# Kernel optimization log

Hardware: AMD Instinct MI355X
Metric: run time of the kernel (lower is better)

## Reference

```python
import jax, jax.numpy as jnp
import numpy as np
from jax import lax

D_MODEL = 1024; N_HEADS = 16; D_FF = 4096
D_INNER = 2048; D_STATE = 16; D_CONV = 4; DT_RANK = 64
B = 4; T = 1024; TF = 512
HD = D_MODEL // N_HEADS


def setup_inputs() -> dict:
    key = jax.random.key(0)
    ks = jax.random.split(key, 24)
    r = lambda i, shape, s=0.02: jax.random.normal(ks[i], shape, jnp.float32) * s
    lengths = jnp.array([512, 384, 448, 320])
    styled_mask = jnp.arange(TF)[None, :] < lengths[:, None]  # True = valid
    inp = {
        'x': jax.random.normal(ks[0], (B, T, D_MODEL), jnp.float32),
        'styled_frames': jax.random.normal(ks[1], (B, TF, D_MODEL), jnp.float32),
        'styled_mask': styled_mask,
        'ln1_g': jnp.ones((D_MODEL,)), 'ln1_b': jnp.zeros((D_MODEL,)),
        'ln2_g': jnp.ones((D_MODEL,)), 'ln2_b': jnp.zeros((D_MODEL,)),
        'ln3_g': jnp.ones((D_MODEL,)), 'ln3_b': jnp.zeros((D_MODEL,)),
        'm_in_w': r(2, (D_MODEL, 2 * D_INNER)),
        'm_conv_w': r(3, (D_INNER, D_CONV), 0.1),
        'm_conv_b': jnp.zeros((D_INNER,)),
        'm_xproj_w': r(4, (D_INNER, DT_RANK + 2 * D_STATE)),
        'm_dt_w': r(5, (DT_RANK, D_INNER), 0.1),
        'm_dt_b': jnp.full((D_INNER,), -4.6),  # softplus -> dt ~ 0.01
        'm_A_log': jnp.log(jnp.broadcast_to(jnp.arange(1, D_STATE + 1, dtype=jnp.float32), (D_INNER, D_STATE))),
        'm_D': jnp.ones((D_INNER,)),
        'm_out_w': r(6, (D_INNER, D_MODEL)),
        'attn_in_w': r(7, (3 * D_MODEL, D_MODEL)),
        'attn_in_b': jnp.zeros((3 * D_MODEL,)),
        'attn_out_w': r(8, (D_MODEL, D_MODEL)),
        'attn_out_b': jnp.zeros((D_MODEL,)),
        'ff_w1': r(9, (D_MODEL, D_FF)),
        'ff_b1': jnp.zeros((D_FF,)),
        'ff_w2': r(10, (D_FF, D_MODEL)),
        'ff_b2': jnp.zeros((D_MODEL,)),
    }
    return inp


def _layer_norm(x, g, b):
    m = x.mean(-1, keepdims=True)
    v = ((x - m) ** 2).mean(-1, keepdims=True)
    return (x - m) / jnp.sqrt(v + 1e-5) * g + b


def _mamba(h, m_in_w, m_conv_w, m_conv_b, m_xproj_w, m_dt_w, m_dt_b, m_A_log, m_D, m_out_w):
    xz = h @ m_in_w                                   # (B,T,2*d_inner)
    xm, z = jnp.split(xz, 2, axis=-1)
    # causal depthwise conv1d
    xt = jnp.pad(xm.transpose(0, 2, 1), ((0, 0), (0, 0), (D_CONV - 1, 0)))  # (B,d_inner,T+pad)
    xc = lax.conv_general_dilated(xt, m_conv_w[:, None, :], (1,), 'VALID',
                                  feature_group_count=D_INNER,
                                  dimension_numbers=('NCH', 'OIH', 'NCH'))
    xc = jax.nn.silu(xc + m_conv_b[None, :, None]).transpose(0, 2, 1)       # (B,T,d_inner)
    x_dbl = xc @ m_xproj_w
    dt, Bs, Cs = jnp.split(x_dbl, [DT_RANK, DT_RANK + D_STATE], axis=-1)
    dt = jax.nn.softplus(dt @ m_dt_w + m_dt_b)        # (B,T,d_inner)
    A = -jnp.exp(m_A_log)                             # (d_inner,d_state)

    def step(hs, inp):
        dt_t, B_t, C_t, u_t = inp                     # (B,d_inner),(B,d_state),(B,d_state),(B,d_inner)
        dA = jnp.exp(dt_t[:, :, None] * A)            # (B,d_inner,d_state)
        hs = dA * hs + dt_t[:, :, None] * B_t[:, None, :] * u_t[:, :, None]
        y = jnp.einsum('bds,bs->bd', hs, C_t)
        return hs, y

    h0 = jnp.zeros((xc.shape[0], D_INNER, D_STATE), xc.dtype)
    inputs = (dt.transpose(1, 0, 2), Bs.transpose(1, 0, 2), Cs.transpose(1, 0, 2), xc.transpose(1, 0, 2))
    hT, ys = lax.scan(step, h0, inputs)
    y = ys.transpose(1, 0, 2) + xc * m_D
    y = y * jax.nn.silu(z)
    return y @ m_out_w, hT


def _cross_attn(q_in, kv_in, valid_mask, in_w, in_b, out_w, out_b):
    d = D_MODEL
    q = q_in @ in_w[:d].T + in_b[:d]
    k = kv_in @ in_w[d:2 * d].T + in_b[d:2 * d]
    v = kv_in @ in_w[2 * d:].T + in_b[2 * d:]
    q = q.reshape(q.shape[0], q.shape[1], N_HEADS, HD)
    k = k.reshape(k.shape[0], k.shape[1], N_HEADS, HD)
    v = v.reshape(v.shape[0], v.shape[1], N_HEADS, HD)
    scores = jnp.einsum('bqhd,bkhd->bhqk', q, k) / np.sqrt(HD)
    scores = jnp.where(valid_mask[:, None, None, :], scores, jnp.finfo(scores.dtype).min)
    attn = jax.nn.softmax(scores, axis=-1)
    o = jnp.einsum('bhqk,bkhd->bqhd', attn, v).reshape(q_in.shape)
    return o @ out_w.T + out_b


def reference(x, styled_frames, styled_mask,
              ln1_g, ln1_b, ln2_g, ln2_b, ln3_g, ln3_b,
              m_in_w, m_conv_w, m_conv_b, m_xproj_w, m_dt_w, m_dt_b, m_A_log, m_D, m_out_w,
              attn_in_w, attn_in_b, attn_out_w, attn_out_b,
              ff_w1, ff_b1, ff_w2, ff_b2):
    h = _layer_norm(x, ln1_g, ln1_b)
    h_mamba, new_state = _mamba(h, m_in_w, m_conv_w, m_conv_b, m_xproj_w, m_dt_w, m_dt_b, m_A_log, m_D, m_out_w)
    x = x + h_mamba
    h = _layer_norm(x, ln2_g, ln2_b)
    x = x + _cross_attn(h, styled_frames, styled_mask, attn_in_w, attn_in_b, attn_out_w, attn_out_b)
    h = _layer_norm(x, ln3_g, ln3_b)
    ff = jax.nn.gelu(h @ ff_w1 + ff_b1, approximate=False) @ ff_w2 + ff_b2
    x = x + ff
    return x, new_state
```

## Files before the change

### kernel.cpp

```cpp
#include <hip/hip_runtime.h>
#include <hip/hip_bf16.h>
#include <cstdint>

using bf16 = __hip_bfloat16;

typedef __attribute__((ext_vector_type(8))) short short8;
typedef __attribute__((ext_vector_type(4))) float floatx4;

__device__ __forceinline__ float b2f(bf16 h) { return __bfloat162float(h); }
__device__ __forceinline__ bf16 f2b(float f) { return __float2bfloat16(f); }
__device__ __forceinline__ float uitf(unsigned u) { union { unsigned u; float f; } c; c.u = u; return c.f; }

__device__ __forceinline__ void async16(const bf16* g, bf16* l) {
    __builtin_amdgcn_global_load_lds(
        (const __attribute__((address_space(1))) uint32_t*)(const void*)g,
        (__attribute__((address_space(3))) uint32_t*)(void*)l, 16, 0, 0);
}

__global__ void lens_flag_kernel(const unsigned char* __restrict__ mask,
                                 const unsigned int* __restrict__ ln1g_raw,
                                 int* __restrict__ hdr) {
    __shared__ int cnt[4];
    int tid = threadIdx.x;
    if (tid < 4) cnt[tid] = 0;
    __syncthreads();
    unsigned char b0 = mask[0], b1 = mask[1];
    int width = (b1 == 0) ? 4 : ((b0 == 1) ? 1 : 2);
    if (width == 4) {
        const unsigned int* m = (const unsigned int*)mask;
        for (int i = tid; i < 2048; i += 256) if (m[i] != 0u) atomicAdd(&cnt[i >> 9], 1);
    } else if (width == 2) {
        const unsigned short* m = (const unsigned short*)mask;
        for (int i = tid; i < 2048; i += 256) if (m[i] != 0u) atomicAdd(&cnt[i >> 9], 1);
    } else {
        for (int i = tid; i < 2048; i += 256) if (mask[i] != 0u) atomicAdd(&cnt[i >> 9], 1);
    }
    __syncthreads();
    if (tid < 4) hdr[tid] = cnt[tid];
    if (tid == 4) hdr[4] = (ln1g_raw[0] == 0x3F800000u) ? 1 : 0;
}

__global__ void convert_kernel(const void* __restrict__ src, bf16* __restrict__ dst, int n,
                               const int* __restrict__ flagp) {
    int i = blockIdx.x * 256 + threadIdx.x;
    if (i >= n) return;
    if (*flagp) dst[i] = f2b(((const float*)src)[i]);
    else        dst[i] = ((const bf16*)src)[i];
}

struct SmallSrcs { const void* p[15]; };
__global__ void convert_smalls_kernel(SmallSrcs s, bf16* __restrict__ dst,
                                      const int* __restrict__ flagp) {
    const int ends[16] = {0, 1024, 2048, 3072, 4096, 5120, 6144, 14336, 16384, 18432,
                          51200, 53248, 56320, 57344, 61440, 62464};
    int i = blockIdx.x * 256 + threadIdx.x;
    if (i >= 62464) return;
    int seg = 0;
    #pragma unroll
    for (int k = 1; k < 16; ++k) if (i >= ends[k]) seg = k;
    int local = i - ends[seg];
    const void* sp = s.p[seg];
    if (*flagp) dst[i] = f2b(((const float*)sp)[local]);
    else        dst[i] = ((const bf16*)sp)[local];
}

__global__ void transpose_any(const void* __restrict__ src, bf16* __restrict__ dst,
                              int R, int C, const int* __restrict__ flagp) {
    __shared__ bf16 tile[32][33];
    bool f32 = (*flagp != 0);
    int bx = blockIdx.x * 32, by = blockIdx.y * 32;
    int tx = threadIdx.x;
    for (int i = threadIdx.y; i < 32; i += 8) {
        int y = by + i, x = bx + tx;
        if (y < R && x < C) {
            size_t idx = (size_t)y * C + x;
            tile[i][tx] = f32 ? f2b(((const float*)src)[idx]) : ((const bf16*)src)[idx];
        }
    }
    __syncthreads();
    for (int i = threadIdx.y; i < 32; i += 8) {
        int yo = bx + i, xo = by + tx;
        if (yo < C && xo < R) dst[(size_t)yo * R + xo] = tile[tx][i];
    }
}

__global__ void vtrans_kernel(const bf16* __restrict__ v, bf16* __restrict__ vt) {
    __shared__ bf16 t[32][33];
    int kc = blockIdx.x * 32, dc = blockIdx.y * 32;
    int bh = blockIdx.z; int b = bh >> 4, h = bh & 15;
    int tx = threadIdx.x;
    for (int i = threadIdx.y; i < 32; i += 8)
        t[i][tx] = v[(size_t)(b * 512 + kc + i) * 1024 + h * 64 + dc + tx];
    __syncthreads();
    for (int i = threadIdx.y; i < 32; i += 8)
        vt[(size_t)(bh * 64 + dc + i) * 512 + kc + tx] = t[tx][i];
}

__global__ __launch_bounds__(256) void ln_kernel(const bf16* __restrict__ x, const bf16* __restrict__ g,
                                                 const bf16* __restrict__ bb, bf16* __restrict__ out) {
    int row = blockIdx.x, tid = threadIdx.x;
    const bf16* xr = x + (size_t)row * 1024;
    float v[4];
    {
        uint2 raw = *(const uint2*)(xr + tid * 4);
        v[0] = uitf(raw.x << 16); v[1] = uitf(raw.x & 0xffff0000u);
        v[2] = uitf(raw.y << 16); v[3] = uitf(raw.y & 0xffff0000u);
    }
    float sum = v[0] + v[1] + v[2] + v[3];
    float sq = v[0]*v[0] + v[1]*v[1] + v[2]*v[2] + v[3]*v[3];
    for (int off = 32; off; off >>= 1) { sum += __shfl_xor(sum, off); sq += __shfl_xor(sq, off); }
    __shared__ float wsm[8];
    int wave = tid >> 6;
    if ((tid & 63) == 0) { wsm[wave * 2] = sum; wsm[wave * 2 + 1] = sq; }
    __syncthreads();
    sum = wsm[0] + wsm[2] + wsm[4] + wsm[6];
    sq  = wsm[1] + wsm[3] + wsm[5] + wsm[7];
    float mean = sum * (1.f / 1024.f);
    float var = sq * (1.f / 1024.f) - mean * mean;
    float rstd = rsqrtf(var + 1e-5f);
    bf16* orow = out + (size_t)row * 1024;
    #pragma unroll
    for (int c = 0; c < 4; ++c) {
        int col = tid * 4 + c;
        orow[col] = f2b((v[c] - mean) * rstd * b2f(g[col]) + b2f(bb[col]));
    }
}

__global__ __launch_bounds__(256) void gemm_bt(
    const bf16* __restrict__ A, int lda,
    const bf16* __restrict__ Bt, int ldb,
    void* __restrict__ Cp, int ldc, int c_f32,
    int M, int N, int K,
    const bf16* __restrict__ bias,
    const bf16* __restrict__ res, int ldres,
    int act)
{
    __shared__ __align__(16) bf16 As[2][128 * 32];
    __shared__ __align__(16) bf16 Bs[2][128 * 32];
    const int tid = threadIdx.x;
    const int lane = tid & 63;
    const int wave = tid >> 6;
    const int wr = (wave >> 1) * 64;
    const int wc = (wave & 1) * 64;
    const int lrow = lane & 15;
    const int quad = lane >> 4;
    const int m0 = blockIdx.y * 128;
    const int n0 = blockIdx.x * 128;

    const int r0 = tid >> 2;
    const int c0 = (tid & 3) << 3;

    floatx4 acc[4][4];
    #pragma unroll
    for (int i = 0; i < 4; ++i)
        #pragma unroll
        for (int j = 0; j < 4; ++j) acc[i][j] = (floatx4){0.f, 0.f, 0.f, 0.f};

    const int n1 = n0 + r0, n2 = n0 + r0 + 64;
    const bool fullN = (n0 + 128 <= N);
    const bool bok1 = n1 < N, bok2 = n2 < N;
    const int4 z4 = {0, 0, 0, 0};

    const bf16* Ag1 = A + (size_t)(m0 + r0) * lda + c0;
    const bf16* Ag2 = A + (size_t)(m0 + r0 + 64) * lda + c0;
    const bf16* Bg1 = Bt + (size_t)n1 * ldb + c0;
    const bf16* Bg2 = Bt + (size_t)n2 * ldb + c0;

    auto stage = [&](int buf, int k0) {
        bf16* AsW = &As[buf][tid * 8];
        bf16* BsW = &Bs[buf][tid * 8];
        async16(Ag1 + k0, AsW);
        async16(Ag2 + k0, AsW + 64 * 32);
        if (fullN) {
            async16(Bg1 + k0, BsW);
            async16(Bg2 + k0, BsW + 64 * 32);
        } else {
            *(int4*)BsW              = bok1 ? *(const int4*)(Bg1 + k0) : z4;
            *(int4*)(BsW + 64 * 32)  = bok2 ? *(const int4*)(Bg2 + k0) : z4;
        }
    };

    const int nt = K >> 5;
    stage(0, 0);
    __syncthreads();
    for (int t = 0; t < nt; ++t) {
        const int cur = t & 1;
        if (t + 1 < nt) stage(cur ^ 1, (t + 1) << 5);
        short8 af[4], bfr[4];
        #pragma unroll
        for (int i = 0; i < 4; ++i) af[i]  = *(const short8*)&As[cur][(wr + i * 16 + lrow) * 32 + quad * 8];
        #pragma unroll
        for (int j = 0; j < 4; ++j) bfr[j] = *(const short8*)&Bs[cur][(wc + j * 16 + lrow) * 32 + quad * 8];
        #pragma unroll
        for (int i = 0; i < 4; ++i)
            #pragma unroll
            for (int j = 0; j < 4; ++j)
                acc[i][j] = __builtin_amdgcn_mfma_f32_16x16x32_bf16(af[i], bfr[j], acc[i][j], 0, 0, 0);
        __syncthreads();
    }

    #pragma unroll
    for (int j = 0; j < 4; ++j) {
        int col = n0 + wc + j * 16 + lrow;
        if (col >= N) continue;
        float bv = bias ? b2f(bias[col]) : 0.f;
        #pragma unroll
        for (int i = 0; i < 4; ++i) {
            #pragma unroll
            for (int r = 0; r < 4; ++r) {
                int row = m0 + wr + i * 16 + quad * 4 + r;
                float v = acc[i][j][r] + bv;
                if (act == 1)      v = 0.5f * v * (1.f + erff(v * 0.70710678118f));
                else if (act == 2) v = (v > 15.f) ? v : log1pf(__expf(v));
                if (res) v += b2f(res[(size_t)row * ldres + col]);
                if (c_f32) ((float*)Cp)[(size_t)row * ldc + col] = v;
                else       ((bf16*)Cp)[(size_t)row * ldc + col] = f2b(v);
            }
        }
    }
}

__global__ __launch_bounds__(256) void conv_silu_kernel(const bf16* __restrict__ xz, const bf16* __restrict__ cw,
                                                        const bf16* __restrict__ cb, bf16* __restrict__ xc) {
    int idx = blockIdx.x * 256 + threadIdx.x;
    int d = idx & 2047;
    int row = idx >> 11;
    int t = row & 1023;
    int base = row - t;
    float acc = b2f(cb[d]);
    #pragma unroll
    for (int j = 0; j < 4; ++j) {
        int tt = t - 3 + j;
        if (tt >= 0) acc += b2f(xz[(size_t)(base + tt) * 4096 + d]) * b2f(cw[d * 4 + j]);
    }
    xc[idx] = f2b(acc * (1.f / (1.f + __expf(-acc))));
}

__global__ __launch_bounds__(256) void scan_part1(
    const bf16* __restrict__ dt, const bf16* __restrict__ xc, const bf16* __restrict__ xdbl,
    const bf16* __restrict__ A_log, float* __restrict__ Pb, float* __restrict__ qb)
{
    __shared__ float smB[128][20];
    const int tid = threadIdx.x;
    const int dgrp = blockIdx.x, c = blockIdx.y, b = blockIdx.z;
    const int dl = tid >> 1, sh = tid & 1;
    const int d = (dgrp << 7) + dl;
    const size_t rowbase = (size_t)b * 1024 + (size_t)c * 128;

    {
        int r = tid >> 1, q = tid & 1;
        short8 raw = *(const short8*)(xdbl + (rowbase + r) * 96 + 64 + q * 8);
        #pragma unroll
        for (int j = 0; j < 8; ++j) smB[r][q * 8 + j] = b2f(((const bf16*)&raw)[j]);
    }
    __syncthreads();

    float A2[8], h[8];
    #pragma unroll
    for (int s = 0; s < 8; ++s) {
        A2[s] = -__expf(b2f(A_log[d * 16 + sh * 8 + s])) * 1.44269504f;
        h[s] = 0.f;
    }
    float dtsum = 0.f;
    const bf16* dtp = dt + rowbase * 2048 + d;
    const bf16* up  = xc + rowbase * 2048 + d;
    for (int tc = 0; tc < 128; tc += 8) {
        float dtv[8], uv[8];
        #pragma unroll
        for (int i = 0; i < 8; ++i) {
            dtv[i] = b2f(dtp[(size_t)(tc + i) * 2048]);
            uv[i]  = b2f(up[(size_t)(tc + i) * 2048]);
        }
        #pragma unroll
        for (int i = 0; i < 8; ++i) {
            float dtf = dtv[i];
            dtsum += dtf;
            float w = dtf * uv[i];
            float4 B0 = *(const float4*)&smB[tc + i][sh * 8];
            float4 B1 = *(const float4*)&smB[tc + i][sh * 8 + 4];
            float Bv[8] = {B0.x, B0.y, B0.z, B0.w, B1.x, B1.y, B1.z, B1.w};
            #pragma unroll
            for (int s = 0; s < 8; ++s) {
                float e = __builtin_amdgcn_exp2f(dtf * A2[s]);
                h[s] = fmaf(e, h[s], w * Bv[s]);
            }
        }
    }
    size_t gid = ((size_t)(b * 2048 + d) * 16 + sh * 8) + (size_t)c * 131072;
    float Pv[8];
    #pragma unroll
    for (int s = 0; s < 8; ++s) Pv[s] = __builtin_amdgcn_exp2f(A2[s] * dtsum);
    *(float4*)(Pb + gid)     = *(float4*)&Pv[0];
    *(float4*)(Pb + gid + 4) = *(float4*)&Pv[4];
    *(float4*)(qb + gid)     = *(float4*)&h[0];
    *(float4*)(qb + gid + 4) = *(float4*)&h[4];
}

__global__ __launch_bounds__(256) void scan_stitch(
    const float* __restrict__ Pb, const float* __restrict__ qb,
    float* __restrict__ hs, float* __restrict__ state_out)
{
    int gid = blockIdx.x * 256 + threadIdx.x;
    float h = 0.f;
    #pragma unroll
    for (int c = 0; c < 8; ++c) {
        hs[gid + c * 131072] = h;
        h = Pb[gid + c * 131072] * h + qb[gid + c * 131072];
    }
    state_out[gid] = h;
}

__global__ __launch_bounds__(256) void scan_part3(
    const bf16* __restrict__ dt, const bf16* __restrict__ xc, const bf16* __restrict__ xdbl,
    const bf16* __restrict__ xz, const bf16* __restrict__ A_log, const bf16* __restrict__ Dp,
    const float* __restrict__ hs, bf16* __restrict__ ymul)
{
    __shared__ float smBC[128][36];
    const int tid = threadIdx.x;
    const int dgrp = blockIdx.x, c = blockIdx.y, b = blockIdx.z;
    const int dl = tid >> 1, sh = tid & 1;
    const int d = (dgrp << 7) + dl;
    const size_t rowbase = (size_t)b * 1024 + (size_t)c * 128;

    {
        int r = tid >> 1, q = tid & 1;
        const bf16* src = xdbl + (rowbase + r) * 96 + 64 + q * 16;
        short8 raw0 = *(const short8*)src;
        short8 raw1 = *(const short8*)(src + 8);
        #pragma unroll
        for (int j = 0; j < 8; ++j) {
            smBC[r][q * 16 + j]     = b2f(((const bf16*)&raw0)[j]);
            smBC[r][q * 16 + 8 + j] = b2f(((const bf16*)&raw1)[j]);
        }
    }
    __syncthreads();

    float A2[8], h[8];
    size_t gid = ((size_t)(b * 2048 + d) * 16 + sh * 8) + (size_t)c * 131072;
    {
        float4 h0 = *(const float4*)(hs + gid);
        float4 h1 = *(const float4*)(hs + gid + 4);
        h[0] = h0.x; h[1] = h0.y; h[2] = h0.z; h[3] = h0.w;
        h[4] = h1.x; h[5] = h1.y; h[6] = h1.z; h[7] = h1.w;
    }
    #pragma unroll
    for (int s = 0; s < 8; ++s)
        A2[s] = -__expf(b2f(A_log[d * 16 + sh * 8 + s])) * 1.44269504f;
    const float Dv = b2f(Dp[d]);
    const bf16* dtp = dt + rowbase * 2048 + d;
    const bf16* up  = xc + rowbase * 2048 + d;
    const bf16* zp  = xz + rowbase * 4096 + 2048 + d;
    bf16* yp = ymul + rowbase * 2048 + d;
    for (int tc = 0; tc < 128; tc += 8) {
        float dtv[8], uv[8], zv[8];
        #pragma unroll
        for (int i = 0; i < 8; ++i) {
            dtv[i] = b2f(dtp[(size_t)(tc + i) * 2048]);
            uv[i]  = b2f(up[(size_t)(tc + i) * 2048]);
            zv[i]  = b2f(zp[(size_t)(tc + i) * 4096]);
        }
        #pragma unroll
        for (int i = 0; i < 8; ++i) {
            float dtf = dtv[i], uf = uv[i];
            float w = dtf * uf;
            float4 B0 = *(const float4*)&smBC[tc + i][sh * 8];
            float4 B1 = *(const float4*)&smBC[tc + i][sh * 8 + 4];
            float4 C0 = *(const float4*)&smBC[tc + i][16 + sh * 8];
            float4 C1 = *(const float4*)&smBC[tc + i][16 + sh * 8 + 4];
            float Bv[8] = {B0.x, B0.y, B0.z, B0.w, B1.x, B1.y, B1.z, B1.w};
            float Cv[8] = {C0.x, C0.y, C0.z, C0.w, C1.x, C1.y, C1.z, C1.w};
            float y = 0.f;
            #pragma unroll
            for (int s = 0; s < 8; ++s) {
                float e = __builtin_amdgcn_exp2f(dtf * A2[s]);
                h[s] = fmaf(e, h[s], w * Bv[s]);
                y = fmaf(h[s], Cv[s], y);
            }
            y += __shfl_xor(y, 1);
            float z = zv[i];
            float sig = __builtin_amdgcn_rcpf(1.f + __builtin_amdgcn_exp2f(-1.44269504f * z));
            float o = (y + uf * Dv) * (z * sig);
            if (sh == 0) yp[(size_t)(tc + i) * 2048] = f2b(o);
        }
    }
}

__global__ __launch_bounds__(256) void attn_mfma(
    const bf16* __restrict__ qb, const bf16* __restrict__ kb, const bf16* __restrict__ vt,
    const int* __restrict__ lens, bf16* __restrict__ ob)
{
    const int qt = blockIdx.x, h = blockIdx.y, b = blockIdx.z;
    const int tid = threadIdx.x;
    const int wave = tid >> 6;
    const int lane = tid & 63;
    const int l15 = lane & 15;
    const int quad = lane >> 4;
    const int len = lens[b];

    __shared__ __align__(16) bf16 Ps[32][520];
    __shared__ float red_sh[4][32];

    short8 aq[2][2];
    const bf16* qbase = qb + (size_t)(b * 1024 + qt * 32 + l15) * 1024 + h * 64 + quad * 8;
    #pragma unroll
    for (int mt = 0; mt < 2; ++mt)
        #pragma unroll
        for (int ks = 0; ks < 2; ++ks)
            aq[mt][ks] = *(const short8*)(qbase + (size_t)mt * 16 * 1024 + ks * 32);

    floatx4 accs[2][8];
    #pragma unroll
    for (int mt = 0; mt < 2; ++mt)
        #pragma unroll
        for (int nt = 0; nt < 8; ++nt) accs[mt][nt] = (floatx4){0.f, 0.f, 0.f, 0.f};

    const bf16* kbase = kb + (size_t)(b * 512 + wave * 128 + l15) * 1024 + h * 64 + quad * 8;
    #pragma unroll
    for (int nt = 0; nt < 8; ++nt) {
        short8 bk0 = *(const short8*)(kbase + (size_t)nt * 16 * 1024);
        short8 bk1 = *(const short8*)(kbase + (size_t)nt * 16 * 1024 + 32);
        #pragma unroll
        for (int mt = 0; mt < 2; ++mt) {
            accs[mt][nt] = __builtin_amdgcn_mfma_f32_16x16x32_bf16(aq[mt][0], bk0, accs[mt][nt], 0, 0, 0);
            accs[mt][nt] = __builtin_amdgcn_mfma_f32_16x16x32_bf16(aq[mt][1], bk1, accs[mt][nt], 0, 0, 0);
        }
    }

    float pm[2][4];
    #pragma unroll
    for (int mt = 0; mt < 2; ++mt)
        #pragma unroll
        for (int r = 0; r < 4; ++r) pm[mt][r] = -1e30f;
    #pragma unroll
    for (int mt = 0; mt < 2; ++mt)
        #pragma unroll
        for (int nt = 0; nt < 8; ++nt) {
            int col = wave * 128 + nt * 16 + l15;
            bool ok = col < len;
            #pragma unroll
            for (int r = 0; r < 4; ++r) {
                float s = ok ? accs[mt][nt][r] * 0.125f : -1e30f;
                accs[mt][nt][r] = s;
                pm[mt][r] = fmaxf(pm[mt][r], s);
            }
        }
    #pragma unroll
    for (int off = 1; off < 16; off <<= 1)
        #pragma unroll
        for (int mt = 0; mt < 2; ++mt)
            #pragma unroll
            for (int r = 0; r < 4; ++r) pm[mt][r] = fmaxf(pm[mt][r], __shfl_xor(pm[mt][r], off));
    if (l15 == 0)
        #pragma unroll
        for (int mt = 0; mt < 2; ++mt)
            #pragma unroll
            for (int r = 0; r < 4; ++r) red_sh[wave][mt * 16 + quad * 4 + r] = pm[mt][r];
    __syncthreads();
    float rowmax[2][4];
    #pragma unroll
    for (int mt = 0; mt < 2; ++mt)
        #pragma unroll
        for (int r = 0; r < 4; ++r) {
            int row = mt * 16 + quad * 4 + r;
            rowmax[mt][r] = fmaxf(fmaxf(red_sh[0][row], red_sh[1][row]),
                                  fmaxf(red_sh[2][row], red_sh[3][row]));
        }
    __syncthreads();

    float ps[2][4] = {{0.f, 0.f, 0.f, 0.f}, {0.f, 0.f, 0.f, 0.f}};
    #pragma unroll
    for (int mt = 0; mt < 2; ++mt)
        #pragma unroll
        for (int nt = 0; nt < 8; ++nt)
            #pragma unroll
            for (int r = 0; r < 4; ++r) {
                float p = __expf(accs[mt][nt][r] - rowmax[mt][r]);
                accs[mt][nt][r] = p;
                ps[mt][r] += p;
            }
    #pragma unroll
    for (int off = 1; off < 16; off <<= 1)
        #pragma unroll
        for (int mt = 0; mt < 2; ++mt)
            #pragma unroll
            for (int r = 0; r < 4; ++r) ps[mt][r] += __shfl_xor(ps[mt][r], off);
    if (l15 == 0)
        #pragma unroll
        for (int mt = 0; mt < 2; ++mt)
            #pragma unroll
            for (int r = 0; r < 4; ++r) red_sh[wave][mt * 16 + quad * 4 + r] = ps[mt][r];
    #pragma unroll
    for (int mt = 0; mt < 2; ++mt)
        #pragma unroll
        for (int nt = 0; nt < 8; ++nt)
            #pragma unroll
            for (int r = 0; r < 4; ++r)
                Ps[mt * 16 + quad * 4 + r][wave * 128 + nt * 16 + l15] = f2b(accs[mt][nt][r]);
    __syncthreads();
    float rowsum[2][4];
    #pragma unroll
    for (int mt = 0; mt < 2; ++mt)
        #pragma unroll
        for (int r = 0; r < 4; ++r) {
            int row = mt * 16 + quad * 4 + r;
            rowsum[mt][r] = red_sh[0][row] + red_sh[1][row] + red_sh[2][row] + red_sh[3][row];
        }

    floatx4 acco[2];
    acco[0] = (floatx4){0.f, 0.f, 0.f, 0.f};
    acco[1] = (floatx4){0.f, 0.f, 0.f, 0.f};
    const bf16* vtbase = vt + (size_t)((b * 16 + h) * 64 + wave * 16 + l15) * 512 + quad * 8;
    #pragma unroll
    for (int kc = 0; kc < 16; ++kc) {
        short8 bv = *(const short8*)(vtbase + kc * 32);
        short8 ap0 = *(const short8*)&Ps[l15][kc * 32 + quad * 8];
        short8 ap1 = *(const short8*)&Ps[16 + l15][kc * 32 + quad * 8];
        acco[0] = __builtin_amdgcn_mfma_f32_16x16x32_bf16(ap0, bv, acco[0], 0, 0, 0);
        acco[1] = __builtin_amdgcn_mfma_f32_16x16x32_bf16(ap1, bv, acco[1], 0, 0, 0);
    }

    #pragma unroll
    for (int mt = 0; mt < 2; ++mt)
        #pragma unroll
        for (int r = 0; r < 4; ++r) {
            int row = b * 1024 + qt * 32 + mt * 16 + quad * 4 + r;
            int col = h * 64 + wave * 16 + l15;
            ob[(size_t)row * 1024 + col] = f2b(acco[mt][r] / rowsum[mt][r]);
        }
}

extern "C" void kernel_launch(void* const* d_in, const int* in_sizes, int n_in,
                              void* d_out, int out_size, void* d_ws, size_t ws_size,
                              hipStream_t stream) {
    bf16* W = (bf16*)d_ws;
    int* hdr = (int*)d_ws;
    const int* flagp = hdr + 4;
    const size_t CV_X     = 32;
    const size_t CV_ST    = CV_X    + 4194304;
    const size_t CV_AIW   = CV_ST   + 2097152;
    const size_t CV_AOW   = CV_AIW  + 3145728;
    const size_t CV_SM    = CV_AOW  + 1048576;
    const size_t WT_IN    = CV_SM   + 62464;
    const size_t WT_XPROJ = WT_IN   + 4194304;
    const size_t WT_DT    = WT_XPROJ + 196608;
    const size_t WT_OUT   = WT_DT   + 131072;
    const size_t WT_FF1   = WT_OUT  + 2097152;
    const size_t WT_FF2   = WT_FF1  + 4194304;
    const size_t HB   = WT_FF2 + 4194304;
    const size_t XZ   = HB     + 4194304;
    const size_t XC   = XZ     + 16777216;
    const size_t XDBL = XC     + 8388608;
    const size_t DTB  = XDBL   + 393216;
    const size_t YM   = DTB    + 8388608;
    const size_t X2  = HB;
    const size_t HB2 = DTB;
    const size_t Qb  = XZ;
    const size_t Kb  = XZ + 4194304;
    const size_t Vb  = XZ + 6291456;
    const size_t AO  = XC;
    const size_t VT  = XC + 4194304;
    const size_t X3  = YM;
    const size_t HB3 = DTB;
    const size_t FFH = XZ;
    float* Pb = (float*)(W + HB);
    float* qbuf = Pb + 1048576;
    float* hstart = (float*)(W + WT_IN);
    const size_t S_LN1G = 0, S_LN1B = 1024, S_LN2G = 2048, S_LN2B = 3072, S_LN3G = 4096, S_LN3B = 5120;
    const size_t S_CW = 6144, S_CB = 14336, S_DTB = 16384, S_AL = 18432, S_D = 51200;
    const size_t S_AIB = 53248, S_AOB = 56320, S_FB1 = 57344, S_FB2 = 61440;

    float* out = (float*)d_out;
    float* state_out = out + (size_t)4 * 1024 * 1024;

    lens_flag_kernel<<<1, 256, 0, stream>>>((const unsigned char*)d_in[2],
                                            (const unsigned int*)d_in[3], hdr);
    convert_kernel<<<16384, 256, 0, stream>>>(d_in[0],  W + CV_X,   4194304, flagp);
    convert_kernel<<<8192,  256, 0, stream>>>(d_in[1],  W + CV_ST,  2097152, flagp);
    convert_kernel<<<12288, 256, 0, stream>>>(d_in[18], W + CV_AIW, 3145728, flagp);
    convert_kernel<<<4096,  256, 0, stream>>>(d_in[20], W + CV_AOW, 1048576, flagp);
    SmallSrcs ss;
    ss.p[0] = d_in[3];  ss.p[1] = d_in[4];  ss.p[2] = d_in[5];  ss.p[3] = d_in[6];
    ss.p[4] = d_in[7];  ss.p[5] = d_in[8];  ss.p[6] = d_in[10]; ss.p[7] = d_in[11];
    ss.p[8] = d_in[14]; ss.p[9] = d_in[15]; ss.p[10] = d_in[16]; ss.p[11] = d_in[19];
    ss.p[12] = d_in[21]; ss.p[13] = d_in[23]; ss.p[14] = d_in[25];
    convert_smalls_kernel<<<245, 256, 0, stream>>>(ss, W + CV_SM, flagp);

    dim3 tb(32, 8);
    transpose_any<<<dim3(128, 32), tb, 0, stream>>>(d_in[9],  W + WT_IN,    1024, 4096, flagp);
    transpose_any<<<dim3(3, 64),   tb, 0, stream>>>(d_in[12], W + WT_XPROJ, 2048, 96,   flagp);
    transpose_any<<<dim3(64, 2),   tb, 0, stream>>>(d_in[13], W + WT_DT,    64,   2048, flagp);
    transpose_any<<<dim3(32, 64),  tb, 0, stream>>>(d_in[17], W + WT_OUT,   2048, 1024, flagp);
    transpose_any<<<dim3(128, 32), tb, 0, stream>>>(d_in[22], W + WT_FF1,   1024, 4096, flagp);
    transpose_any<<<dim3(32, 128), tb, 0, stream>>>(d_in[24], W + WT_FF2,   4096, 1024, flagp);

    auto gemm = [&](const bf16* A, int lda, const bf16* Bt, int ldb, void* C, int ldc, int c_f32,
                    int M, int N, int K, const bf16* bias, const bf16* res, int ldres, int act) {
        dim3 grid((N + 127) / 128, M / 128);
        gemm_bt<<<grid, 256, 0, stream>>>(A, lda, Bt, ldb, C, ldc, c_f32, M, N, K, bias, res, ldres, act);
    };

    ln_kernel<<<4096, 256, 0, stream>>>(W + CV_X, W + CV_SM + S_LN1G, W + CV_SM + S_LN1B, W + HB);
    gemm(W + HB, 1024, W + WT_IN, 1024, W + XZ, 4096, 0, 4096, 4096, 1024, nullptr, nullptr, 0, 0);
    conv_silu_kernel<<<32768, 256, 0, stream>>>(W + XZ, W + CV_SM + S_CW, W + CV_SM + S_CB, W + XC);
    gemm(W + XC, 2048, W + WT_XPROJ, 2048, W + XDBL, 96, 0, 4096, 96, 2048, nullptr, nullptr, 0, 0);
    gemm(W + XDBL, 96, W + WT_DT, 64, W + DTB, 2048, 0, 4096, 2048, 64, W + CV_SM + S_DTB, nullptr, 0, 2);
    scan_part1<<<dim3(16, 8, 4), 256, 0, stream>>>(W + DTB, W + XC, W + XDBL, W + CV_SM + S_AL, Pb, qbuf);
    scan_stitch<<<512, 256, 0, stream>>>(Pb, qbuf, hstart, state_out);
    scan_part3<<<dim3(16, 8, 4), 256, 0, stream>>>(W + DTB, W + XC, W + XDBL, W + XZ,
                                                   W + CV_SM + S_AL, W + CV_SM + S_D, hstart, W + YM);
    gemm(W + YM, 2048, W + WT_OUT, 2048, W + X2, 1024, 0, 4096, 1024, 2048, nullptr, W + CV_X, 1024, 0);

    ln_kernel<<<4096, 256, 0, stream>>>(W + X2, W + CV_SM + S_LN2G, W + CV_SM + S_LN2B, W + HB2);
    gemm(W + HB2, 1024, W + CV_AIW, 1024, W + Qb, 1024, 0, 4096, 1024, 1024, W + CV_SM + S_AIB, nullptr, 0, 0);
    gemm(W + CV_ST, 1024, W + CV_AIW + 1048576, 1024, W + Kb, 1024, 0, 2048, 1024, 1024, W + CV_SM + S_AIB + 1024, nullptr, 0, 0);
    gemm(W + CV_ST, 1024, W + CV_AIW + 2097152, 1024, W + Vb, 1024, 0, 2048, 1024, 1024, W + CV_SM + S_AIB + 2048, nullptr, 0, 0);
    vtrans_kernel<<<dim3(16, 2, 64), tb, 0, stream>>>(W + Vb, W + VT);
    attn_mfma<<<dim3(32, 16, 4), 256, 0, stream>>>(W + Qb, W + Kb, W + VT, hdr, W + AO);
    gemm(W + AO, 1024, W + CV_AOW, 1024, W + X3, 1024, 0, 4096, 1024, 1024, W + CV_SM + S_AOB, W + X2, 1024, 0);

    ln_kernel<<<4096, 256, 0, stream>>>(W + X3, W + CV_SM + S_LN3G, W + CV_SM + S_LN3B, W + HB3);
    gemm(W + HB3, 1024, W + WT_FF1, 1024, W + FFH, 4096, 0, 4096, 4096, 1024, W + CV_SM + S_FB1, nullptr, 0, 1);
    gemm(W + FFH, 4096, W + WT_FF2, 4096, out, 1024, 1, 4096, 1024, 4096, W + CV_SM + S_FB2, W + X3, 1024, 0);
}
```

Before: 1.026 ms.

## Triple-buffer GEMM LDS with vmcnt waits and XOR-swizzled chunk layout

Moves the bf16 GEMM's full-N path from double buffering to a three-stage LDS ring. Global-to-LDS loads are issued two tiles ahead, and each step uses a partial s_waitcnt vmcnt plus one barrier instead of two __syncthreads. It also XOR-swizzles the 16-byte K-chunk position by row on both the write side and the fragment-read side, to cut LDS bank conflicts. This costs 50% more shared memory (48KB), which may lower occupancy, and the hand-written vmcnt counting is fragile; the partial-N path becomes a simpler single-buffered loop.

Measured after the change: 1.024 ms. No clear change (-0.2%).

```diff
diff --git a/kernel.cpp b/kernel.cpp
--- a/kernel.cpp
+++ b/kernel.cpp
@@ -135,8 +135,8 @@
     const bf16* __restrict__ res, int ldres,
     int act)
 {
-    __shared__ __align__(16) bf16 As[2][128 * 32];
-    __shared__ __align__(16) bf16 Bs[2][128 * 32];
+    __shared__ __align__(16) bf16 As[3][128 * 32];
+    __shared__ __align__(16) bf16 Bs[3][128 * 32];
     const int tid = threadIdx.x;
     const int lane = tid & 63;
     const int wave = tid >> 6;
@@ -148,7 +148,7 @@
     const int n0 = blockIdx.x * 128;
 
     const int r0 = tid >> 2;
-    const int c0 = (tid & 3) << 3;
+    const int c0 = (((tid & 3) ^ ((r0 >> 1) & 3)) << 3);
 
     floatx4 acc[4][4];
     #pragma unroll
@@ -166,37 +166,63 @@
     const bf16* Bg1 = Bt + (size_t)n1 * ldb + c0;
     const bf16* Bg2 = Bt + (size_t)n2 * ldb + c0;
 
-    auto stage = [&](int buf, int k0) {
-        bf16* AsW = &As[buf][tid * 8];
-        bf16* BsW = &Bs[buf][tid * 8];
-        async16(Ag1 + k0, AsW);
-        async16(Ag2 + k0, AsW + 64 * 32);
-        if (fullN) {
+    const int chsw = ((quad ^ ((lrow >> 1) & 3)) << 3);
+    const int nt = K >> 5;
+
+    if (fullN) {
+        auto stage = [&](int buf, int k0) {
+            bf16* AsW = &As[buf][tid * 8];
+            bf16* BsW = &Bs[buf][tid * 8];
+            async16(Ag1 + k0, AsW);
+            async16(Ag2 + k0, AsW + 64 * 32);
             async16(Bg1 + k0, BsW);
             async16(Bg2 + k0, BsW + 64 * 32);
-        } else {
+        };
+        stage(0, 0);
+        if (nt > 1) stage(1, 32);
+        int cur = 0;
+        for (int t = 0; t < nt; ++t) {
+            if (t + 1 < nt) asm volatile("s_waitcnt vmcnt(4)" ::: "memory");
+            else            asm volatile("s_waitcnt vmcnt(0)" ::: "memory");
+            __builtin_amdgcn_s_barrier();
+            __builtin_amdgcn_sched_barrier(0);
+            if (t + 2 < nt) {
+                int nb = cur + 2; if (nb >= 3) nb -= 3;
+                stage(nb, (t + 2) << 5);
+            }
+            short8 af[4], bfr[4];
+            #pragma unroll
+            for (int i = 0; i < 4; ++i) af[i]  = *(const short8*)&As[cur][(wr + i * 16 + lrow) * 32 + chsw];
+            #pragma unroll
+            for (int j = 0; j < 4; ++j) bfr[j] = *(const short8*)&Bs[cur][(wc + j * 16 + lrow) * 32 + chsw];
+            #pragma unroll
+            for (int i = 0; i < 4; ++i)
+                #pragma unroll
+                for (int j = 0; j < 4; ++j)
+                    acc[i][j] = __builtin_amdgcn_mfma_f32_16x16x32_bf16(af[i], bfr[j], acc[i][j], 0, 0, 0);
+            if (++cur == 3) cur = 0;
+        }
+    } else {
+        bf16* AsW = &As[0][tid * 8];
+        bf16* BsW = &Bs[0][tid * 8];
+        for (int k0 = 0; k0 < K; k0 += 32) {
+            __syncthreads();
+            async16(Ag1 + k0, AsW);
+            async16(Ag2 + k0, AsW + 64 * 32);
             *(int4*)BsW              = bok1 ? *(const int4*)(Bg1 + k0) : z4;
             *(int4*)(BsW + 64 * 32)  = bok2 ? *(const int4*)(Bg2 + k0) : z4;
-        }
-    };
-
-    const int nt = K >> 5;
-    stage(0, 0);
-    __syncthreads();
-    for (int t = 0; t < nt; ++t) {
-        const int cur = t & 1;
-        if (t + 1 < nt) stage(cur ^ 1, (t + 1) << 5);
-        short8 af[4], bfr[4];
-        #pragma unroll
-        for (int i = 0; i < 4; ++i) af[i]  = *(const short8*)&As[cur][(wr + i * 16 + lrow) * 32 + quad * 8];
-        #pragma unroll
-        for (int j = 0; j < 4; ++j) bfr[j] = *(const short8*)&Bs[cur][(wc + j * 16 + lrow) * 32 + quad * 8];
-        #pragma unroll
-        for (int i = 0; i < 4; ++i)
-            #pragma unroll
-            for (int j = 0; j < 4; ++j)
-                acc[i][j] = __builtin_amdgcn_mfma_f32_16x16x32_bf16(af[i], bfr[j], acc[i][j], 0, 0, 0);
-        __syncthreads();
+            __syncthreads();
+            short8 af[4], bfr[4];
+            #pragma unroll
+            for (int i = 0; i < 4; ++i) af[i]  = *(const short8*)&As[0][(wr + i * 16 + lrow) * 32 + chsw];
+            #pragma unroll
+            for (int j = 0; j < 4; ++j) bfr[j] = *(const short8*)&Bs[0][(wc + j * 16 + lrow) * 32 + chsw];
+            #pragma unroll
+            for (int i = 0; i < 4; ++i)
+                #pragma unroll
+                for (int j = 0; j < 4; ++j)
+                    acc[i][j] = __builtin_amdgcn_mfma_f32_16x16x32_bf16(af[i], bfr[j], acc[i][j], 0, 0, 0);
+        }
     }
 
     #pragma unroll
```
